# Kernel optimization log

Hardware: AMD Instinct MI355X
Metric: run time of the kernel (lower is better)

## Reference

```python
import jax, jax.numpy as jnp
import numpy as np

SEQ_LEN, BATCH, INPUT_SIZE, HIDDEN = 512, 64, 256, 1024

def setup_inputs() -> dict:
    key = jax.random.key(0)
    ks = jax.random.split(key, 17)
    s_x = 1.0 / np.sqrt(INPUT_SIZE)
    s_h = 1.0 / np.sqrt(HIDDEN)
    def lin(k, out_d, in_d, s):
        kw, kb = jax.random.split(k)
        W = jax.random.uniform(kw, (out_d, in_d), jnp.float32, -s, s)
        b = jax.random.uniform(kb, (out_d,), jnp.float32, -s, s)
        return W, b
    x = jax.random.normal(ks[0], (SEQ_LEN, BATCH, INPUT_SIZE), jnp.float32)
    Wfx, bfx = lin(ks[1], HIDDEN, INPUT_SIZE, s_x)
    Wix, bix = lin(ks[2], HIDDEN, INPUT_SIZE, s_x)
    Wgx, bgx = lin(ks[3], HIDDEN, INPUT_SIZE, s_x)
    Wox, box = lin(ks[4], HIDDEN, INPUT_SIZE, s_x)
    Wfh, bfh = lin(ks[5], HIDDEN, HIDDEN, s_h)
    Wih, bih = lin(ks[6], HIDDEN, HIDDEN, s_h)
    Wgh, bgh = lin(ks[7], HIDDEN, HIDDEN, s_h)
    Woh, boh = lin(ks[8], HIDDEN, HIDDEN, s_h)
    return {"x": x, "Wfx": Wfx, "bfx": bfx, "Wix": Wix, "bix": bix,
            "Wgx": Wgx, "bgx": bgx, "Wox": Wox, "box": box,
            "Wfh": Wfh, "bfh": bfh, "Wih": Wih, "bih": bih,
            "Wgh": Wgh, "bgh": bgh, "Woh": Woh, "boh": boh}

def reference(x, Wfx, bfx, Wix, bix, Wgx, bgx, Wox, box,
              Wfh, bfh, Wih, bih, Wgh, bgh, Woh, boh):
    B, H = x.shape[1], Wfh.shape[0]
    # precompute input projections for all 4 gates across the whole sequence
    xf = jnp.einsum('sbi,hi->sbh', x, Wfx) + bfx
    xi = jnp.einsum('sbi,hi->sbh', x, Wix) + bix
    xg = jnp.einsum('sbi,hi->sbh', x, Wgx) + bgx
    xo = jnp.einsum('sbi,hi->sbh', x, Wox) + box

    def step(carry, gates_t):
        h, c = carry
        gf, gi, gg, go = gates_t
        f = jax.nn.sigmoid(h @ Wfh.T + bfh + gf)
        i1 = jax.nn.sigmoid(h @ Wih.T + bih + gi)
        i2 = jnp.tanh(h @ Wgh.T + bgh + gg)
        c = c * f + i1 * i2
        h = jnp.tanh(c) * jax.nn.sigmoid(h @ Woh.T + boh + go)
        return (h, c), h

    h0 = jnp.zeros((B, H), x.dtype)  # self.h/self.c zeros broadcast to batch
    c0 = jnp.zeros((B, H), x.dtype)
    (h, c), h_seq = jax.lax.scan(step, (h0, c0), (xf, xi, xg, xo))
    return h_seq, h[None], c[None]  # (S,B,H), (1,B,H), (1,B,H)
```

## Files before the change

kernel.cpp:

```cpp
#include <hip/hip_runtime.h>


#define SEQ   512
#define BATCH 64
#define ISZ   256
#define HID   1024
#define NCOL  4096
#define KH    1024
#define KTOT  1280
#define NKS   40
#define NKSH  32
#define NBLK  128
#define NSUB  2
#define WSUB  (NKS * 512)

typedef __attribute__((ext_vector_type(8))) short bf16x8;
typedef __attribute__((ext_vector_type(4))) float f32x4;
typedef unsigned short u16;
typedef unsigned int u32;
typedef unsigned long long u64;

#define WSW_ELEMS  ((size_t)NCOL * KTOT)
#define XB_ELEMS   ((size_t)SEQ * BATCH * ISZ)
#define HBUF_ELEMS ((size_t)2 * BATCH * HID)

__device__ __forceinline__ u16 f2bf(float f) {
    union { float f; unsigned int u; } c; c.f = f;
    unsigned int u = c.u;
    u += 0x7fffu + ((u >> 16) & 1u);
    return (u16)(u >> 16);
}

struct WPtrs { const float* Wh[4]; const float* Wx[4]; };

__global__ __launch_bounds__(256) void build_w(WPtrs wp, u16* __restrict__ Wsw) {
    size_t did = (size_t)blockIdx.x * 256 + threadIdx.x;
    if (did >= WSW_ELEMS / 8) return;
    int lane = (int)(did & 63);
    size_t rest = did >> 6;
    int ks = (int)(rest % NKS);
    int cg = (int)(rest / NKS);
    int nl = lane & 15, q = lane >> 4;
    int col = cg * 16 + nl;
    int g = col & 3, n = col >> 2;
    int k0 = ks * 32 + q * 8;
    const float* src = (k0 < KH) ? wp.Wh[g] + (size_t)n * KH + k0
                                 : wp.Wx[g] + (size_t)n * ISZ + (k0 - KH);
    u16 tmp[8];
#pragma unroll
    for (int j = 0; j < 8; ++j) tmp[j] = f2bf(src[j]);
    *(bf16x8*)(Wsw + did * 8) = *(const bf16x8*)tmp;
}

__global__ __launch_bounds__(256) void conv_x(const float* __restrict__ x,
                                              u16* __restrict__ xb,
                                              u32* __restrict__ flags) {
    if (blockIdx.x == 0 && threadIdx.x < NBLK)
        __hip_atomic_store(&flags[threadIdx.x], 0u, __ATOMIC_RELAXED,
                           __HIP_MEMORY_SCOPE_AGENT);
    size_t i = (size_t)blockIdx.x * 256 + threadIdx.x;
    float4 v0 = ((const float4*)x)[i * 2];
    float4 v1 = ((const float4*)x)[i * 2 + 1];
    u16 tmp[8] = { f2bf(v0.x), f2bf(v0.y), f2bf(v0.z), f2bf(v0.w),
                   f2bf(v1.x), f2bf(v1.y), f2bf(v1.z), f2bf(v1.w) };
    *(bf16x8*)(xb + i * 8) = *(const bf16x8*)tmp;
}

struct SeqP {
    const u16* xb;
    const float* bfh; const float* bfx;
    const float* bih; const float* bix;
    const float* bgh; const float* bgx;
    const float* boh; const float* box;
    const u16* Wsw;
    u16* hbuf;
    float* out;
    u32* flags;
};

__global__ __launch_bounds__(256, 1) void lstm_seq(SeqP p) {
    __shared__ __attribute__((aligned(16))) u16   Wl[NSUB * WSUB];
    __shared__ __attribute__((aligned(16))) float Gsh[NSUB][4][16][20];
    __shared__ __attribute__((aligned(8)))  u16 hsh[BATCH][8];

    const int t    = threadIdx.x;
    const int lane = t & 63;
    const int w    = t >> 6;
    const int cg2  = blockIdx.x;
    const int ml   = lane & 15;
    const int q    = lane >> 4;
    const int arow = w * 16 + ml;

    {
        const float4* src = (const float4*)(p.Wsw + (size_t)cg2 * (NSUB * WSUB));
        float4* dst = (float4*)Wl;
#pragma unroll
        for (int i = 0; i < 20; ++i) dst[t + 256 * i] = src[t + 256 * i];
    }

    const int row2 = lane >> 2;
    const int hl   = lane & 3;
    const int bb   = w * 16 + row2;
    float Bf[NSUB], Bi[NSUB], Bg[NSUB], Bo[NSUB], c[NSUB];
#pragma unroll
    for (int sub = 0; sub < NSUB; ++sub) {
        int nn = cg2 * 8 + sub * 4 + hl;
        Bf[sub] = p.bfh[nn] + p.bfx[nn];
        Bi[sub] = p.bih[nn] + p.bix[nn];
        Bg[sub] = p.bgh[nn] + p.bgx[nn];
        Bo[sub] = p.boh[nn] + p.box[nn];
        c[sub]  = 0.f;
    }

    const u16* Wlp = Wl + lane * 8;
    union AFrag { u64 d[2]; bf16x8 v; };

    __syncthreads();

    for (int s = 0; s < SEQ; ++s) {
        const u64* hrd = (const u64*)(p.hbuf + (size_t)(s & 1) * (BATCH * HID));
        u64*       hwr = (u64*)(p.hbuf + (size_t)((s + 1) & 1) * (BATCH * HID));

        f32x4 acc[NSUB][4];
#pragma unroll
        for (int sub = 0; sub < NSUB; ++sub)
#pragma unroll
            for (int j = 0; j < 4; ++j) acc[sub][j] = f32x4{0.f, 0.f, 0.f, 0.f};

        {
            const u16* Xp = p.xb + ((size_t)s * BATCH + arow) * ISZ + q * 8;
#pragma unroll
            for (int ks = 0; ks < 8; ++ks) {
                bf16x8 a  = *(const bf16x8*)(Xp + ks * 32);
                bf16x8 b0 = *(const bf16x8*)(Wlp + (size_t)(NKSH + ks) * 512);
                bf16x8 b1 = *(const bf16x8*)(Wlp + WSUB + (size_t)(NKSH + ks) * 512);
                acc[0][ks & 3] = __builtin_amdgcn_mfma_f32_16x16x32_bf16(a, b0, acc[0][ks & 3], 0, 0, 0);
                acc[1][ks & 3] = __builtin_amdgcn_mfma_f32_16x16x32_bf16(a, b1, acc[1][ks & 3], 0, 0, 0);
            }
        }

        if (s > 0) {
            if (w == 0) {
                const u64* f2 = (const u64*)p.flags + lane;
                for (;;) {
                    u64 v = __hip_atomic_load(f2, __ATOMIC_RELAXED,
                                              __HIP_MEMORY_SCOPE_AGENT);
                    int ok = ((u32)v >= (u32)s) && ((u32)(v >> 32) >= (u32)s);
                    if (__all(ok)) break;
                    __builtin_amdgcn_s_sleep(2);
                }
            }
            __syncthreads();
            __builtin_amdgcn_fence(__ATOMIC_ACQUIRE, "workgroup");

            const u64* Ap = hrd + (size_t)arow * 2;
#pragma unroll 8
            for (int ks = 0; ks < NKSH; ++ks) {
                const u64* Ab = Ap + (size_t)(ks * 4 + q) * 128;
                AFrag a;
                a.d[0] = __hip_atomic_load(Ab,     __ATOMIC_RELAXED, __HIP_MEMORY_SCOPE_AGENT);
                a.d[1] = __hip_atomic_load(Ab + 1, __ATOMIC_RELAXED, __HIP_MEMORY_SCOPE_AGENT);
                bf16x8 b0 = *(const bf16x8*)(Wlp + (size_t)ks * 512);
                bf16x8 b1 = *(const bf16x8*)(Wlp + WSUB + (size_t)ks * 512);
                acc[0][ks & 3] = __builtin_amdgcn_mfma_f32_16x16x32_bf16(a.v, b0, acc[0][ks & 3], 0, 0, 0);
                acc[1][ks & 3] = __builtin_amdgcn_mfma_f32_16x16x32_bf16(a.v, b1, acc[1][ks & 3], 0, 0, 0);
            }
        }

#pragma unroll
        for (int sub = 0; sub < NSUB; ++sub) {
            f32x4 av = (acc[sub][0] + acc[sub][1]) + (acc[sub][2] + acc[sub][3]);
#pragma unroll
            for (int r = 0; r < 4; ++r) Gsh[sub][w][q * 4 + r][ml] = av[r];
        }
        __syncthreads();

        float hv[NSUB];
#pragma unroll
        for (int sub = 0; sub < NSUB; ++sub) {
            float4 gv = *(const float4*)&Gsh[sub][w][row2][hl * 4];
            float fg = 1.f / (1.f + __expf(-(gv.x + Bf[sub])));
            float ig = 1.f / (1.f + __expf(-(gv.y + Bi[sub])));
            float gg = 1.f - 2.f / (1.f + __expf(2.f * (gv.z + Bg[sub])));
            float og = 1.f / (1.f + __expf(-(gv.w + Bo[sub])));
            c[sub] = c[sub] * fg + ig * gg;
            hv[sub] = (1.f - 2.f / (1.f + __expf(2.f * c[sub]))) * og;
            hsh[bb][sub * 4 + hl] = f2bf(hv[sub]);
        }
        __syncthreads();

        if (t < 128) {
            u64 v = ((const u64*)hsh)[t];
            __hip_atomic_store(hwr + (size_t)cg2 * 128 + t, v,
                               __ATOMIC_RELAXED, __HIP_MEMORY_SCOPE_AGENT);
        }
        __builtin_amdgcn_fence(__ATOMIC_RELEASE, "workgroup");
        __builtin_amdgcn_s_waitcnt(0);
        __syncthreads();
        if (t == 0)
            __hip_atomic_store(&p.flags[cg2], (u32)(s + 1), __ATOMIC_RELAXED,
                               __HIP_MEMORY_SCOPE_AGENT);

#pragma unroll
        for (int sub = 0; sub < NSUB; ++sub) {
            int nn = cg2 * 8 + sub * 4 + hl;
            p.out[(size_t)s * (BATCH * HID) + (size_t)bb * HID + nn] = hv[sub];
            if (s == SEQ - 1) {
                p.out[(size_t)SEQ * (BATCH * HID) + (size_t)bb * HID + nn] = hv[sub];
                p.out[(size_t)SEQ * (BATCH * HID) + (BATCH * HID) + (size_t)bb * HID + nn] = c[sub];
            }
        }
    }
}

extern "C" void kernel_launch(void* const* d_in, const int* in_sizes, int n_in,
                              void* d_out, int out_size, void* d_ws, size_t ws_size,
                              hipStream_t stream) {
    WPtrs wp;
    wp.Wx[0] = (const float*)d_in[1];  wp.Wx[1] = (const float*)d_in[3];
    wp.Wx[2] = (const float*)d_in[5];  wp.Wx[3] = (const float*)d_in[7];
    wp.Wh[0] = (const float*)d_in[9];  wp.Wh[1] = (const float*)d_in[11];
    wp.Wh[2] = (const float*)d_in[13]; wp.Wh[3] = (const float*)d_in[15];

    u16* Wsw  = (u16*)d_ws;
    u16* xb   = Wsw + WSW_ELEMS;
    u16* hbuf = xb + XB_ELEMS;
    u32* flags = (u32*)(hbuf + HBUF_ELEMS);

    SeqP p;
    p.xb   = xb;
    p.bfx  = (const float*)d_in[2];   p.bix  = (const float*)d_in[4];
    p.bgx  = (const float*)d_in[6];   p.box  = (const float*)d_in[8];
    p.bfh  = (const float*)d_in[10];  p.bih  = (const float*)d_in[12];
    p.bgh  = (const float*)d_in[14];  p.boh  = (const float*)d_in[16];
    p.Wsw  = Wsw;
    p.hbuf = hbuf;
    p.out  = (float*)d_out;
    p.flags = flags;

    build_w<<<dim3(2560), 256, 0, stream>>>(wp, Wsw);
    conv_x<<<dim3(4096), 256, 0, stream>>>((const float*)d_in[0], xb, flags);
    lstm_seq<<<dim3(NBLK), 256, 0, stream>>>(p);
}
```

Measured before the change: 3.844 ms.

## Overlap next-step input projection with barrier and write h directly per thread

Moves the input-projection MFMA work for step s+1 ahead of the release barrier, so it runs while other blocks finish step s instead of on the critical path after the flag wait. The hidden state is no longer staged in shared memory: each thread packs its two bf16 h values into one 32-bit atomic store, with the weight layout in build_w permuted to match the new interleaving. This drops one __syncthreads and the staging copy. Output stores become nontemporal. The risk is a longer gap before the flag is published, since the flag is now written only after the next step's x-part, which may delay the other blocks that wait on it.

```diff
diff --git a/kernel.cpp b/kernel.cpp
--- a/kernel.cpp
+++ b/kernel.cpp
@@ -44,11 +44,16 @@
     int col = cg * 16 + nl;
     int g = col & 3, n = col >> 2;
     int k0 = ks * 32 + q * 8;
-    const float* src = (k0 < KH) ? wp.Wh[g] + (size_t)n * KH + k0
-                                 : wp.Wx[g] + (size_t)n * ISZ + (k0 - KH);
     u16 tmp[8];
-#pragma unroll
-    for (int j = 0; j < 8; ++j) tmp[j] = f2bf(src[j]);
+    if (k0 < KH) {
+        const float* src = wp.Wh[g] + (size_t)n * KH + k0;
+#pragma unroll
+        for (int j = 0; j < 8; ++j) tmp[j] = f2bf(src[(j >> 1) + 4 * (j & 1)]);
+    } else {
+        const float* src = wp.Wx[g] + (size_t)n * ISZ + (k0 - KH);
+#pragma unroll
+        for (int j = 0; j < 8; ++j) tmp[j] = f2bf(src[j]);
+    }
     *(bf16x8*)(Wsw + did * 8) = *(const bf16x8*)tmp;
 }
 
@@ -78,10 +83,25 @@
     u32* flags;
 };
 
+#define XPART(S) do {                                                              \
+    _Pragma("unroll")                                                              \
+    for (int sub_ = 0; sub_ < NSUB; ++sub_)                                        \
+        _Pragma("unroll")                                                          \
+        for (int jj_ = 0; jj_ < 4; ++jj_) acc[sub_][jj_] = f32x4{0.f,0.f,0.f,0.f}; \
+    const u16* Xp_ = p.xb + ((size_t)(S) * BATCH + arow) * ISZ + q * 8;            \
+    _Pragma("unroll")                                                              \
+    for (int ks_ = 0; ks_ < 8; ++ks_) {                                            \
+        bf16x8 a_  = *(const bf16x8*)(Xp_ + ks_ * 32);                             \
+        bf16x8 b0_ = *(const bf16x8*)(Wlp + (size_t)(NKSH + ks_) * 512);           \
+        bf16x8 b1_ = *(const bf16x8*)(Wlp + WSUB + (size_t)(NKSH + ks_) * 512);    \
+        acc[0][ks_ & 3] = __builtin_amdgcn_mfma_f32_16x16x32_bf16(a_, b0_, acc[0][ks_ & 3], 0, 0, 0); \
+        acc[1][ks_ & 3] = __builtin_amdgcn_mfma_f32_16x16x32_bf16(a_, b1_, acc[1][ks_ & 3], 0, 0, 0); \
+    }                                                                              \
+} while (0)
+
 __global__ __launch_bounds__(256, 1) void lstm_seq(SeqP p) {
     __shared__ __attribute__((aligned(16))) u16   Wl[NSUB * WSUB];
     __shared__ __attribute__((aligned(16))) float Gsh[NSUB][4][16][20];
-    __shared__ __attribute__((aligned(8)))  u16 hsh[BATCH][8];
 
     const int t    = threadIdx.x;
     const int lane = t & 63;
@@ -117,28 +137,10 @@
 
     __syncthreads();
 
+    f32x4 acc[NSUB][4];
+    XPART(0);
+
     for (int s = 0; s < SEQ; ++s) {
-        const u64* hrd = (const u64*)(p.hbuf + (size_t)(s & 1) * (BATCH * HID));
-        u64*       hwr = (u64*)(p.hbuf + (size_t)((s + 1) & 1) * (BATCH * HID));
-
-        f32x4 acc[NSUB][4];
-#pragma unroll
-        for (int sub = 0; sub < NSUB; ++sub)
-#pragma unroll
-            for (int j = 0; j < 4; ++j) acc[sub][j] = f32x4{0.f, 0.f, 0.f, 0.f};
-
-        {
-            const u16* Xp = p.xb + ((size_t)s * BATCH + arow) * ISZ + q * 8;
-#pragma unroll
-            for (int ks = 0; ks < 8; ++ks) {
-                bf16x8 a  = *(const bf16x8*)(Xp + ks * 32);
-                bf16x8 b0 = *(const bf16x8*)(Wlp + (size_t)(NKSH + ks) * 512);
-                bf16x8 b1 = *(const bf16x8*)(Wlp + WSUB + (size_t)(NKSH + ks) * 512);
-                acc[0][ks & 3] = __builtin_amdgcn_mfma_f32_16x16x32_bf16(a, b0, acc[0][ks & 3], 0, 0, 0);
-                acc[1][ks & 3] = __builtin_amdgcn_mfma_f32_16x16x32_bf16(a, b1, acc[1][ks & 3], 0, 0, 0);
-            }
-        }
-
         if (s > 0) {
             if (w == 0) {
                 const u64* f2 = (const u64*)p.flags + lane;
@@ -153,6 +155,7 @@
             __syncthreads();
             __builtin_amdgcn_fence(__ATOMIC_ACQUIRE, "workgroup");
 
+            const u64* hrd = (const u64*)(p.hbuf + (size_t)(s & 1) * (BATCH * HID));
             const u64* Ap = hrd + (size_t)arow * 2;
 #pragma unroll 8
             for (int ks = 0; ks < NKSH; ++ks) {
@@ -185,30 +188,36 @@
             float og = 1.f / (1.f + __expf(-(gv.w + Bo[sub])));
             c[sub] = c[sub] * fg + ig * gg;
             hv[sub] = (1.f - 2.f / (1.f + __expf(2.f * c[sub]))) * og;
-            hsh[bb][sub * 4 + hl] = f2bf(hv[sub]);
-        }
-        __syncthreads();
-
-        if (t < 128) {
-            u64 v = ((const u64*)hsh)[t];
-            __hip_atomic_store(hwr + (size_t)cg2 * 128 + t, v,
+        }
+
+        if (s < SEQ - 1) {
+            u32* hwr32 = (u32*)p.hbuf + (size_t)((s + 1) & 1) * (BATCH * HID / 2);
+            u32 pk = (u32)f2bf(hv[0]) | ((u32)f2bf(hv[1]) << 16);
+            __hip_atomic_store(hwr32 + (size_t)cg2 * 256 + bb * 4 + hl, pk,
                                __ATOMIC_RELAXED, __HIP_MEMORY_SCOPE_AGENT);
         }
-        __builtin_amdgcn_fence(__ATOMIC_RELEASE, "workgroup");
-        __builtin_amdgcn_s_waitcnt(0);
-        __syncthreads();
-        if (t == 0)
-            __hip_atomic_store(&p.flags[cg2], (u32)(s + 1), __ATOMIC_RELAXED,
-                               __HIP_MEMORY_SCOPE_AGENT);
 
 #pragma unroll
         for (int sub = 0; sub < NSUB; ++sub) {
             int nn = cg2 * 8 + sub * 4 + hl;
-            p.out[(size_t)s * (BATCH * HID) + (size_t)bb * HID + nn] = hv[sub];
+            __builtin_nontemporal_store(hv[sub],
+                &p.out[(size_t)s * (BATCH * HID) + (size_t)bb * HID + nn]);
             if (s == SEQ - 1) {
-                p.out[(size_t)SEQ * (BATCH * HID) + (size_t)bb * HID + nn] = hv[sub];
-                p.out[(size_t)SEQ * (BATCH * HID) + (BATCH * HID) + (size_t)bb * HID + nn] = c[sub];
+                __builtin_nontemporal_store(hv[sub],
+                    &p.out[(size_t)SEQ * (BATCH * HID) + (size_t)bb * HID + nn]);
+                __builtin_nontemporal_store(c[sub],
+                    &p.out[(size_t)SEQ * (BATCH * HID) + (BATCH * HID) + (size_t)bb * HID + nn]);
             }
+        }
+
+        if (s < SEQ - 1) {
+            XPART(s + 1);
+            __builtin_amdgcn_fence(__ATOMIC_RELEASE, "workgroup");
+            __builtin_amdgcn_s_waitcnt(0);
+            __syncthreads();
+            if (t == 0)
+                __hip_atomic_store(&p.flags[cg2], (u32)(s + 1), __ATOMIC_RELAXED,
+                                   __HIP_MEMORY_SCOPE_AGENT);
         }
     }
 }
```

Result: slower. 5.109 ms (+32.9%).
